# Kernel tuning notes

Measured on AMD Instinct MI355X. Metric: run time of the kernel, lower is better.

The kernel has to match this reference:

```python
import jax, jax.numpy as jnp
import numpy as np

B, L, D, H, E, NL, K = 32, 256, 256, 256, 8, 4, 4


def setup_inputs() -> dict:
    key = jax.random.key(0)
    ks = jax.random.split(key, 8)
    sc = 1.0 / float(np.sqrt(H))
    x = jax.random.normal(ks[0], (B, L, D), jnp.float32)
    conv_w = jax.random.normal(ks[1], (D, 1, K), jnp.float32) * sc
    conv_b = jax.random.normal(ks[2], (D,), jnp.float32) * 0.1
    ln_g = jnp.ones((D,), jnp.float32)
    ln_b = jnp.zeros((D,), jnp.float32)
    W_ih = jax.random.normal(ks[3], (NL, H, D), jnp.float32) * sc
    W_hh = jax.random.normal(ks[4], (NL, H, H), jnp.float32) * sc
    # first layer scaling_init='normal', remaining layers 'ones'
    r0 = jax.random.normal(ks[5], (1, E, D), jnp.float32)
    r = jnp.concatenate([r0, jnp.ones((NL - 1, E, D), jnp.float32)], axis=0)
    s0 = jax.random.normal(ks[6], (1, E, H), jnp.float32)
    s = jnp.concatenate([s0, jnp.ones((NL - 1, E, H), jnp.float32)], axis=0)
    b = jnp.zeros((NL, H), jnp.float32)
    return dict(x=x, conv_w=conv_w, conv_b=conv_b, ln_g=ln_g, ln_b=ln_b,
                W_ih=W_ih, W_hh=W_hh, r=r, s=s, b=b)


def _layernorm(x, g, b, eps=1e-5):
    m = x.mean(-1, keepdims=True)
    v = ((x - m) ** 2).mean(-1, keepdims=True)
    return (x - m) * jax.lax.rsqrt(v + eps) * g + b


def _rnn_layer(x, W_ih, W_hh, r, s, b):
    # x: (B, E, L, F); batch-ensemble input scaling, shared GEMM, output scaling
    pre = jnp.einsum('belf,hf->belh', x * r[None, :, None, :], W_ih)
    pre = pre * s[None, :, None, :] + b  # (B, E, L, H)

    def step(h, p_t):
        h = jnp.tanh(p_t + jnp.einsum('beh,kh->bek', h, W_hh))
        return h, h

    h0 = jnp.zeros((x.shape[0], x.shape[1], W_hh.shape[0]), x.dtype)
    h_last, ys = jax.lax.scan(step, h0, jnp.moveaxis(pre, 2, 0))  # scan over L
    return jnp.moveaxis(ys, 0, 2), h_last


def reference(x, conv_w, conv_b, ln_g, ln_b, W_ih, W_hh, r, s, b):
    h = _layernorm(x, ln_g, ln_b)                    # (B, L, D)
    h = jnp.transpose(h, (0, 2, 1))                  # (B, D, L)
    # depthwise causal conv1d: pad=(K-1) both sides then [:, :, :L] == left-pad K-1
    h = jax.lax.conv_general_dilated(
        h, conv_w, window_strides=(1,), padding=[(K - 1, 0)],
        dimension_numbers=('NCH', 'OIH', 'NCH'), feature_group_count=D)
    h = h + conv_b[None, :, None]
    h = jnp.transpose(h, (0, 2, 1))                  # (B, L, D)
    h = jnp.broadcast_to(h[:, None], (B, E, L, D))   # replicate across ensemble
    h_last = None
    for i in range(NL):
        h, h_last = _rnn_layer(h, W_ih[i], W_hh[i], r[i], s[i], b[i])
    return h, h_last
```

## Files before the change

### kernel.cpp

```cpp
#include <hip/hip_runtime.h>
#include <hip/hip_bf16.h>
#include <cstdint>


typedef _Float16 f16;
typedef _Float16 f16x4 __attribute__((ext_vector_type(4)));
typedef _Float16 f16x8 __attribute__((ext_vector_type(8)));
typedef float f32x4 __attribute__((ext_vector_type(4)));

__device__ __forceinline__ float tanh_fast(float x) {
  float e = __expf(2.f * x);
  return fmaf(-2.f, __builtin_amdgcn_rcpf(e + 1.f), 1.f);
}

__global__ __launch_bounds__(256) void ln_kernel(
    const float* __restrict__ x, const float* __restrict__ g,
    const float* __restrict__ beta, float* __restrict__ out)
{
  const int row = blockIdx.x;
  const int t = threadIdx.x;
  const float v = x[row * 256 + t];
  __shared__ float red[4];
  float s = v;
  #pragma unroll
  for (int off = 32; off > 0; off >>= 1) s += __shfl_xor(s, off);
  if ((t & 63) == 0) red[t >> 6] = s;
  __syncthreads();
  const float mean = (red[0] + red[1] + red[2] + red[3]) * (1.f / 256.f);
  const float d = v - mean;
  float sq = d * d;
  #pragma unroll
  for (int off = 32; off > 0; off >>= 1) sq += __shfl_xor(sq, off);
  __syncthreads();
  if ((t & 63) == 0) red[t >> 6] = sq;
  __syncthreads();
  const float var = (red[0] + red[1] + red[2] + red[3]) * (1.f / 256.f);
  out[row * 256 + t] = d * rsqrtf(var + 1e-5f) * g[t] + beta[t];
}

__global__ __launch_bounds__(256) void conv_kernel(
    const float* __restrict__ ln, const float* __restrict__ w,
    const float* __restrict__ cb, float* __restrict__ out)
{
  const int l = blockIdx.x & 255;
  const int b = blockIdx.x >> 8;
  const int d = threadIdx.x;
  const float4 wv = *(const float4*)(w + d * 4);
  const float wk[4] = {wv.x, wv.y, wv.z, wv.w};
  float acc = cb[d];
  #pragma unroll
  for (int k = 0; k < 4; ++k) {
    const int ls = l - 3 + k;
    if (ls >= 0) acc = fmaf(ln[((b << 8) + ls) * 256 + d], wk[k], acc);
  }
  out[((b << 8) + l) * 256 + d] = acc;
}

__global__ __launch_bounds__(512) void wcvt_kernel(
    const float* __restrict__ Wi, const float* __restrict__ Wh,
    f16* __restrict__ wi16, f16* __restrict__ wh16)
{
  const int i = blockIdx.x * 512 + threadIdx.x;
  wi16[i] = (f16)Wi[i];
  wh16[i] = (f16)Wh[i];
}

__global__ void zflags_kernel(int* __restrict__ f) { f[threadIdx.x] = 0; }

#define XS_S 264
#define PRE_S 260

__global__ __launch_bounds__(512, 2) void pipe_kernel(
    const float* __restrict__ cvb,
    const f16* __restrict__ wi16,
    const f16* __restrict__ wh16,
    const float* __restrict__ rr,
    const float* __restrict__ ssc,
    const float* __restrict__ bbv,
    f16* __restrict__ ysA,
    f16* __restrict__ ysB,
    float* __restrict__ preG,
    int* __restrict__ flags,
    float* __restrict__ outh,
    float* __restrict__ outl)
{
  __shared__ __align__(16) f16 Xs[16 * XS_S];
  __shared__ __align__(16) f16 hb[2][16 * 256];

  const int tid = threadIdx.x, lane = tid & 63, w = tid >> 6;
  const int n = lane & 15, q = lane >> 4;
  const int blk = blockIdx.x;
  const int l = blk >> 4, g = blk & 15;
  const int fl = tid >> 5;
  const int fc = (tid & 31) << 3;

  const f16* ysin = (((l - 1) & 1) ? ysB : ysA);
  f16* ysout = ((l & 1) ? ysB : ysA);
  float* pblk = preG + (size_t)blk * 65536;
  const int swz = (n & 7) << 4;

  *(f16x8*)((char*)&hb[0][0] + tid * 16) = (f16x8){};
  __syncthreads();

  int cur = 0;

  for (int c = 0; c < 16; ++c) {
    if (l > 0) {
      if (tid == 0) {
        while (__hip_atomic_load(&flags[(l - 1) * 16 + g], __ATOMIC_ACQUIRE,
                                 __HIP_MEMORY_SCOPE_AGENT) < c + 1)
          __builtin_amdgcn_s_sleep(8);
      }
      __syncthreads();
    }

    {
      f16x8 wih[2][8];
      #pragma unroll
      for (int jt = 0; jt < 2; ++jt) {
        const f16* wib = wi16 + l * 65536 + (w * 32 + jt * 16 + n) * 256 + q * 8;
        #pragma unroll
        for (int p = 0; p < 8; ++p) wih[jt][p] = *(const f16x8*)(wib + p * 32);
      }
      for (int s = 0; s < 16; ++s) {
        const int seq = g * 16 + s;
        const int t = c * 16 + fl;
        if (l == 0) {
          const int bb_ = seq >> 3, e = seq & 7;
          const float* rp = rr + e * 256 + fc;
          const f32x4 rva = *(const f32x4*)rp;
          const f32x4 rvb = *(const f32x4*)(rp + 4);
          const float* src = cvb + (size_t)(((bb_ << 8) + t) << 8) + fc;
          const f32x4 x0 = *(const f32x4*)src * rva;
          const f32x4 x1 = *(const f32x4*)(src + 4) * rvb;
          f16x8 v;
          v[0]=(f16)x0.x; v[1]=(f16)x0.y; v[2]=(f16)x0.z; v[3]=(f16)x0.w;
          v[4]=(f16)x1.x; v[5]=(f16)x1.y; v[6]=(f16)x1.z; v[7]=(f16)x1.w;
          *(f16x8*)(Xs + fl * XS_S + fc) = v;
        } else {
          *(f16x8*)(Xs + fl * XS_S + fc) =
              *(const f16x8*)(ysin + (size_t)seq * 65536 + (size_t)t * 256 + fc);
        }
        __syncthreads();

        const int e = seq & 7;
        float sv[2], bv[2];
        sv[0] = ssc[l * 2048 + e * 256 + w * 32 + n];
        sv[1] = ssc[l * 2048 + e * 256 + w * 32 + 16 + n];
        bv[0] = bbv[l * 256 + w * 32 + n];
        bv[1] = bbv[l * 256 + w * 32 + 16 + n];

        f32x4 g00 = {0,0,0,0}, g10 = g00, g01 = g00, g11 = g00;
        #pragma unroll
        for (int p = 0; p < 4; ++p) {
          const f16x8 afa = *(const f16x8*)(Xs + n * XS_S + p * 32 + q * 8);
          const f16x8 afb = *(const f16x8*)(Xs + n * XS_S + (p + 4) * 32 + q * 8);
          g00 = __builtin_amdgcn_mfma_f32_16x16x32_f16(afa, wih[0][p], g00, 0, 0, 0);
          g10 = __builtin_amdgcn_mfma_f32_16x16x32_f16(afa, wih[1][p], g10, 0, 0, 0);
          g01 = __builtin_amdgcn_mfma_f32_16x16x32_f16(afb, wih[0][p + 4], g01, 0, 0, 0);
          g11 = __builtin_amdgcn_mfma_f32_16x16x32_f16(afb, wih[1][p + 4], g11, 0, 0, 0);
        }
        #pragma unroll
        for (int ri = 0; ri < 4; ++ri) {
          const int off = ((q * 4 + ri) * 16 + s) * 256;
          pblk[off + w * 32 + n]      = fmaf(g00[ri] + g01[ri], sv[0], bv[0]);
          pblk[off + w * 32 + 16 + n] = fmaf(g10[ri] + g11[ri], sv[1], bv[1]);
        }
        __syncthreads();
      }
    }

    {
      f16x8 whh[2][8];
      #pragma unroll
      for (int rt = 0; rt < 2; ++rt) {
        const f16* whb = wh16 + l * 65536 + (w * 32 + rt * 16 + n) * 256 + q * 8;
        #pragma unroll
        for (int p = 0; p < 8; ++p) whh[rt][p] = *(const f16x8*)(whb + p * 32);
      }
      f32x4 pc0 = *(const f32x4*)(pblk + n * 256 + w * 32 + q * 4);
      f32x4 pc1 = *(const f32x4*)(pblk + n * 256 + w * 32 + 16 + q * 4);

      for (int t = 0; t < 16; ++t) {
        const int tn = (t + 1) & 15;
        const f32x4 pn0 = *(const f32x4*)(pblk + (tn * 16 + n) * 256 + w * 32 + q * 4);
        const f32x4 pn1 = *(const f32x4*)(pblk + (tn * 16 + n) * 256 + w * 32 + 16 + q * 4);

        f16x8 Bf[8];
        const char* hc = (const char*)&hb[cur][0];
        #pragma unroll
        for (int p = 0; p < 8; ++p)
          Bf[p] = *(const f16x8*)(hc + ((n * 512 + 64 * p + 16 * q) ^ swz));

        f32x4 ac0 = pc0, ac1 = pc1;
        #pragma unroll
        for (int p = 0; p < 8; ++p) {
          ac0 = __builtin_amdgcn_mfma_f32_16x16x32_f16(whh[0][p], Bf[p], ac0, 0, 0, 0);
          ac1 = __builtin_amdgcn_mfma_f32_16x16x32_f16(whh[1][p], Bf[p], ac1, 0, 0, 0);
        }

        char* hn = (char*)&hb[cur ^ 1][0];
        const int tg = c * 16 + t;
        const int seq = g * 16 + n;
        #pragma unroll
        for (int rt = 0; rt < 2; ++rt) {
          const f32x4 a = rt ? ac1 : ac0;
          const float v0 = tanh_fast(a[0]);
          const float v1 = tanh_fast(a[1]);
          const float v2 = tanh_fast(a[2]);
          const float v3 = tanh_fast(a[3]);
          f16x4 hv;
          hv[0] = (f16)v0; hv[1] = (f16)v1; hv[2] = (f16)v2; hv[3] = (f16)v3;
          *(f16x4*)(hn + ((n * 512 + 64 * w + 32 * rt + 8 * q) ^ swz)) = hv;
          const int col = w * 32 + rt * 16 + q * 4;
          if (l < 3) {
            *(f16x4*)(ysout + (size_t)seq * 65536 + (size_t)tg * 256 + col) = hv;
          } else {
            const f32x4 ov = {v0, v1, v2, v3};
            *(f32x4*)(outh + ((size_t)seq * 256 + tg) * 256 + col) = ov;
            if (tg == 255)
              *(f32x4*)(outl + (size_t)seq * 256 + col) = ov;
          }
        }
        __syncthreads();
        cur ^= 1;
        pc0 = pn0; pc1 = pn1;
      }
    }

    if (l < 3 && tid == 0)
      __hip_atomic_fetch_add(&flags[l * 16 + g], 1, __ATOMIC_RELEASE,
                             __HIP_MEMORY_SCOPE_AGENT);
  }
}

__global__ __launch_bounds__(512, 2) void fused_rnn_kernel(
    const float* __restrict__ cvb,
    const f16* __restrict__ wi16,
    const f16* __restrict__ wh16,
    const float* __restrict__ rr,
    const float* __restrict__ ssc,
    const float* __restrict__ bbv,
    f16* __restrict__ ys16,
    float* __restrict__ outh,
    float* __restrict__ outl)
{
  __shared__ __align__(16) f16 Xs[16 * XS_S];
  __shared__ __align__(16) float preb[16 * PRE_S];
  __shared__ __align__(16) f16 hbuf[2 * 272];

  const int tid = threadIdx.x, lane = tid & 63, w = tid >> 6;
  const int n = lane & 15, q = lane >> 4;
  const int seq = blockIdx.x, b = seq >> 3, e = seq & 7;
  const int fl = tid >> 5;
  const int fc = (tid & 31) << 3;

  const int tj = n & 1, tri = (n >> 1) & 3;
  const int hrow = w * 32 + tj * 16 + q * 4 + tri;
  const bool writer = (n < 8);

  f16* myys = ys16 + (size_t)seq * 65536;

  const float* rp = rr + e * 256 + fc;
  const f32x4 rva = *(const f32x4*)rp;
  const f32x4 rvb = *(const f32x4*)(rp + 4);

  for (int layer = 0; layer < 4; ++layer) {
    f16x8 wih[2][8], whh[2][8];
    float sv[2], bv[2];
    #pragma unroll
    for (int jt = 0; jt < 2; ++jt) {
      const int row = w * 32 + jt * 16 + n;
      const f16* wib = wi16 + layer * 65536 + row * 256 + q * 8;
      const f16* whb = wh16 + layer * 65536 + row * 256 + q * 8;
      #pragma unroll
      for (int kc = 0; kc < 8; ++kc) {
        wih[jt][kc] = *(const f16x8*)(wib + kc * 32);
        whh[jt][kc] = *(const f16x8*)(whb + kc * 32);
      }
      sv[jt] = ssc[layer * 2048 + e * 256 + row];
      bv[jt] = bbv[layer * 256 + row];
    }
    if (tid < 68) ((f16x8*)hbuf)[tid] = (f16x8){};

    for (int c = 0; c < 16; ++c) {
      const int lg = (c << 4) + fl;
      if (layer == 0) {
        const float* src = cvb + (size_t)(((b << 8) + lg) << 8) + fc;
        const f32x4 x0 = *(const f32x4*)src * rva;
        const f32x4 x1 = *(const f32x4*)(src + 4) * rvb;
        f16x8 v;
        v[0]=(f16)x0.x; v[1]=(f16)x0.y; v[2]=(f16)x0.z; v[3]=(f16)x0.w;
        v[4]=(f16)x1.x; v[5]=(f16)x1.y; v[6]=(f16)x1.z; v[7]=(f16)x1.w;
        *(f16x8*)(Xs + fl * XS_S + fc) = v;
      } else {
        *(f16x8*)(Xs + fl * XS_S + fc) = *(const f16x8*)(myys + (size_t)lg * 256 + fc);
      }
      __syncthreads();

      {
        f32x4 g00 = {0,0,0,0}, g10 = g00, g01 = g00, g11 = g00;
        #pragma unroll
        for (int p = 0; p < 4; ++p) {
          const f16x8 afa = *(const f16x8*)(Xs + n * XS_S + p * 32 + q * 8);
          const f16x8 afb = *(const f16x8*)(Xs + n * XS_S + (p + 4) * 32 + q * 8);
          g00 = __builtin_amdgcn_mfma_f32_16x16x32_f16(afa, wih[0][p], g00, 0, 0, 0);
          g10 = __builtin_amdgcn_mfma_f32_16x16x32_f16(afa, wih[1][p], g10, 0, 0, 0);
          g01 = __builtin_amdgcn_mfma_f32_16x16x32_f16(afb, wih[0][p + 4], g01, 0, 0, 0);
          g11 = __builtin_amdgcn_mfma_f32_16x16x32_f16(afb, wih[1][p + 4], g11, 0, 0, 0);
        }
        #pragma unroll
        for (int ri = 0; ri < 4; ++ri) {
          preb[(q * 4 + ri) * PRE_S + w * 32 + n]      = fmaf(g00[ri] + g01[ri], sv[0], bv[0]);
          preb[(q * 4 + ri) * PRE_S + w * 32 + 16 + n] = fmaf(g10[ri] + g11[ri], sv[1], bv[1]);
        }
      }
      __syncthreads();

      #pragma unroll 2
      for (int t = 0; t < 16; ++t) {
        const f16* hbp = hbuf + (t & 1) * 272;
        f16x8 Bf[8];
        #pragma unroll
        for (int kc = 0; kc < 8; ++kc)
          Bf[kc] = *(const f16x8*)(hbp + kc * 32 + q * 8);
        f32x4 a00 = *(const f32x4*)(preb + t * PRE_S + w * 32 + q * 4);
        f32x4 a10 = *(const f32x4*)(preb + t * PRE_S + w * 32 + 16 + q * 4);
        f32x4 a01 = {0,0,0,0}, a11 = {0,0,0,0};
        #pragma unroll
        for (int p = 0; p < 4; ++p) {
          a00 = __builtin_amdgcn_mfma_f32_16x16x32_f16(whh[0][p], Bf[p], a00, 0, 0, 0);
          a10 = __builtin_amdgcn_mfma_f32_16x16x32_f16(whh[1][p], Bf[p], a10, 0, 0, 0);
          a01 = __builtin_amdgcn_mfma_f32_16x16x32_f16(whh[0][p + 4], Bf[p + 4], a01, 0, 0, 0);
          a11 = __builtin_amdgcn_mfma_f32_16x16x32_f16(whh[1][p + 4], Bf[p + 4], a11, 0, 0, 0);
        }
        const f32x4 sums = tj ? (a10 + a11) : (a00 + a01);
        const float v = tanh_fast(sums[tri]);
        if (writer) {
          f16* hnext = hbuf + ((t + 1) & 1) * 272;
          hnext[hrow] = (f16)v;
          preb[t * PRE_S + hrow] = v;
          if (layer == 3 && c == 15 && t == 15)
            outl[(size_t)seq * 256 + hrow] = v;
        }
        __syncthreads();
      }

      {
        const float* srow = preb + fl * PRE_S + fc;
        const f32x4 o0 = *(const f32x4*)srow;
        const f32x4 o1 = *(const f32x4*)(srow + 4);
        if (layer < 3) {
          f16x8 hh;
          hh[0]=(f16)o0.x; hh[1]=(f16)o0.y; hh[2]=(f16)o0.z; hh[3]=(f16)o0.w;
          hh[4]=(f16)o1.x; hh[5]=(f16)o1.y; hh[6]=(f16)o1.z; hh[7]=(f16)o1.w;
          *(f16x8*)(myys + (size_t)lg * 256 + fc) = hh;
        } else {
          float* dst = outh + ((size_t)seq * 256 + lg) * 256 + fc;
          *(f32x4*)dst = o0;
          *(f32x4*)(dst + 4) = o1;
        }
      }
      __syncthreads();
    }
  }
}

extern "C" void kernel_launch(void* const* d_in, const int* in_sizes, int n_in,
                              void* d_out, int out_size, void* d_ws, size_t ws_size,
                              hipStream_t stream) {
  const float* x      = (const float*)d_in[0];
  const float* conv_w = (const float*)d_in[1];
  const float* conv_b = (const float*)d_in[2];
  const float* ln_g   = (const float*)d_in[3];
  const float* ln_b   = (const float*)d_in[4];
  const float* W_ih   = (const float*)d_in[5];
  const float* W_hh   = (const float*)d_in[6];
  const float* r      = (const float*)d_in[7];
  const float* s      = (const float*)d_in[8];
  const float* bb     = (const float*)d_in[9];

  float* outh = (float*)d_out;
  float* outl = outh + 16777216;

  const size_t NEED = (size_t)112 << 20;
  if (ws_size >= NEED) {
    f16*   ysA  = (f16*)d_ws;
    f16*   ysB  = (f16*)((char*)d_ws + ((size_t)32 << 20));
    float* cvb  = (float*)((char*)d_ws + ((size_t)64 << 20));
    float* lnb  = (float*)((char*)d_ws + ((size_t)72 << 20));
    f16*   wi16 = (f16*)((char*)d_ws + ((size_t)80 << 20));
    f16*   wh16 = wi16 + 262144;
    float* preG = (float*)((char*)d_ws + ((size_t)81 << 20));
    int*   flags = (int*)((char*)d_ws + ((size_t)97 << 20));

    zflags_kernel<<<1, 64, 0, stream>>>(flags);
    ln_kernel<<<8192, 256, 0, stream>>>(x, ln_g, ln_b, lnb);
    conv_kernel<<<8192, 256, 0, stream>>>(lnb, conv_w, conv_b, cvb);
    wcvt_kernel<<<512, 512, 0, stream>>>(W_ih, W_hh, wi16, wh16);
    pipe_kernel<<<64, 512, 0, stream>>>(cvb, wi16, wh16, r, s, bb,
                                        ysA, ysB, preG, flags, outh, outl);
  } else {
    f16*   ys16 = (f16*)d_ws;
    float* cvb  = (float*)((char*)d_ws + (32u << 20));
    float* lnb  = (float*)((char*)d_ws + (40u << 20));
    f16*   wi16 = (f16*)((char*)d_ws + (48u << 20));
    f16*   wh16 = wi16 + 262144;

    ln_kernel<<<8192, 256, 0, stream>>>(x, ln_g, ln_b, lnb);
    conv_kernel<<<8192, 256, 0, stream>>>(lnb, conv_w, conv_b, cvb);
    wcvt_kernel<<<512, 512, 0, stream>>>(W_ih, W_hh, wi16, wh16);
    fused_rnn_kernel<<<256, 512, 0, stream>>>(cvb, wi16, wh16, r, s, bb,
                                              ys16, outh, outl);
  }
}
```

Measured before the change: 686.6 us.

## Pre-scale fp16 inputs in conv, keep weights resident, batch hidden-state stores per chunk

The conv kernel now also applies the per-ensemble input scaling r and writes an fp16 (B,E,L,D) tensor, so layer 0 no longer rescales and converts inputs on the fly. Inside the pipelined kernel, W_ih and W_hh fragments are loaded into registers once per block, and the input GEMM reads A fragments straight from global memory. That removes the LDS staging buffer and its two barriers per sequence step. Hidden states for a 16-step chunk are kept in a 16-slot LDS ring and written out afterwards with coalesced 16-byte stores, and the ping-pong ys buffers collapse into one. The costs are higher register pressure, final-layer outputs rounded through fp16 before widening to fp32, and a single shared ys buffer that relies on the flag ordering to stay correct.

```diff
diff --git a/kernel.cpp b/kernel.cpp
--- a/kernel.cpp
+++ b/kernel.cpp
@@ -38,9 +38,10 @@
   out[row * 256 + t] = d * rsqrtf(var + 1e-5f) * g[t] + beta[t];
 }
 
-__global__ __launch_bounds__(256) void conv_kernel(
+__global__ __launch_bounds__(256) void convr_kernel(
     const float* __restrict__ ln, const float* __restrict__ w,
-    const float* __restrict__ cb, float* __restrict__ out)
+    const float* __restrict__ cb, const float* __restrict__ rr,
+    f16* __restrict__ xr)
 {
   const int l = blockIdx.x & 255;
   const int b = blockIdx.x >> 8;
@@ -53,6 +54,26 @@
     const int ls = l - 3 + k;
     if (ls >= 0) acc = fmaf(ln[((b << 8) + ls) * 256 + d], wk[k], acc);
   }
+  #pragma unroll
+  for (int e = 0; e < 8; ++e)
+    xr[(size_t)(((b * 8 + e) * 256 + l)) * 256 + d] = (f16)(acc * rr[e * 256 + d]);
+}
+
+__global__ __launch_bounds__(256) void conv_kernel(
+    const float* __restrict__ ln, const float* __restrict__ w,
+    const float* __restrict__ cb, float* __restrict__ out)
+{
+  const int l = blockIdx.x & 255;
+  const int b = blockIdx.x >> 8;
+  const int d = threadIdx.x;
+  const float4 wv = *(const float4*)(w + d * 4);
+  const float wk[4] = {wv.x, wv.y, wv.z, wv.w};
+  float acc = cb[d];
+  #pragma unroll
+  for (int k = 0; k < 4; ++k) {
+    const int ls = l - 3 + k;
+    if (ls >= 0) acc = fmaf(ln[((b << 8) + ls) * 256 + d], wk[k], acc);
+  }
   out[((b << 8) + l) * 256 + d] = acc;
 }
 
@@ -71,38 +92,53 @@
 #define PRE_S 260
 
 __global__ __launch_bounds__(512, 2) void pipe_kernel(
-    const float* __restrict__ cvb,
+    const f16* __restrict__ xr16,
     const f16* __restrict__ wi16,
     const f16* __restrict__ wh16,
-    const float* __restrict__ rr,
     const float* __restrict__ ssc,
     const float* __restrict__ bbv,
-    f16* __restrict__ ysA,
-    f16* __restrict__ ysB,
+    f16* __restrict__ ys,
     float* __restrict__ preG,
     int* __restrict__ flags,
     float* __restrict__ outh,
     float* __restrict__ outl)
 {
-  __shared__ __align__(16) f16 Xs[16 * XS_S];
-  __shared__ __align__(16) f16 hb[2][16 * 256];
+  __shared__ __align__(16) f16 hb[16][4096];
 
   const int tid = threadIdx.x, lane = tid & 63, w = tid >> 6;
   const int n = lane & 15, q = lane >> 4;
   const int blk = blockIdx.x;
   const int l = blk >> 4, g = blk & 15;
-  const int fl = tid >> 5;
-  const int fc = (tid & 31) << 3;
-
-  const f16* ysin = (((l - 1) & 1) ? ysB : ysA);
-  f16* ysout = ((l & 1) ? ysB : ysA);
+  const int swz = (n & 7) << 4;
+  const int fs = tid >> 5;
+  const int fd = (tid & 31) << 3;
+  const int fswz = (fs & 7) << 4;
+
+  const f16* xin = (l == 0) ? xr16 : ys;
   float* pblk = preG + (size_t)blk * 65536;
-  const int swz = (n & 7) << 4;
+
+  f16x8 wih[2][8], whh[2][8];
+  #pragma unroll
+  for (int jt = 0; jt < 2; ++jt) {
+    const f16* wib = wi16 + l * 65536 + (w * 32 + jt * 16 + n) * 256 + q * 8;
+    const f16* whb = wh16 + l * 65536 + (w * 32 + jt * 16 + n) * 256 + q * 8;
+    #pragma unroll
+    for (int p = 0; p < 8; ++p) {
+      wih[jt][p] = *(const f16x8*)(wib + p * 32);
+      whh[jt][p] = *(const f16x8*)(whb + p * 32);
+    }
+  }
+  #pragma unroll
+  for (int jt = 0; jt < 2; ++jt) {
+    #pragma unroll
+    for (int p = 0; p < 8; ++p) {
+      asm volatile("" : "+v"(wih[jt][p]));
+      asm volatile("" : "+v"(whh[jt][p]));
+    }
+  }
 
   *(f16x8*)((char*)&hb[0][0] + tid * 16) = (f16x8){};
   __syncthreads();
-
-  int cur = 0;
 
   for (int c = 0; c < 16; ++c) {
     if (l > 0) {
@@ -114,119 +150,96 @@
       __syncthreads();
     }
 
+    #pragma unroll 2
+    for (int s = 0; s < 16; ++s) {
+      const int seq = g * 16 + s;
+      const f16* xb = xin + (size_t)seq * 65536 + (c * 16 + n) * 256 + q * 8;
+      f32x4 g00 = {0,0,0,0}, g10 = g00, g01 = g00, g11 = g00;
+      #pragma unroll
+      for (int p = 0; p < 4; ++p) {
+        const f16x8 afa = *(const f16x8*)(xb + p * 32);
+        const f16x8 afb = *(const f16x8*)(xb + (p + 4) * 32);
+        g00 = __builtin_amdgcn_mfma_f32_16x16x32_f16(afa, wih[0][p], g00, 0, 0, 0);
+        g10 = __builtin_amdgcn_mfma_f32_16x16x32_f16(afa, wih[1][p], g10, 0, 0, 0);
+        g01 = __builtin_amdgcn_mfma_f32_16x16x32_f16(afb, wih[0][p + 4], g01, 0, 0, 0);
+        g11 = __builtin_amdgcn_mfma_f32_16x16x32_f16(afb, wih[1][p + 4], g11, 0, 0, 0);
+      }
+      const int e = s & 7;
+      const float sv0 = ssc[l * 2048 + e * 256 + w * 32 + n];
+      const float sv1 = ssc[l * 2048 + e * 256 + w * 32 + 16 + n];
+      const float bv0 = bbv[l * 256 + w * 32 + n];
+      const float bv1 = bbv[l * 256 + w * 32 + 16 + n];
+      #pragma unroll
+      for (int ri = 0; ri < 4; ++ri) {
+        const int off = ((q * 4 + ri) * 16 + s) * 256;
+        pblk[off + w * 32 + n]      = fmaf(g00[ri] + g01[ri], sv0, bv0);
+        pblk[off + w * 32 + 16 + n] = fmaf(g10[ri] + g11[ri], sv1, bv1);
+      }
+    }
+
+    f32x4 pc0 = *(const f32x4*)(pblk + n * 256 + w * 32 + q * 4);
+    f32x4 pc1 = *(const f32x4*)(pblk + n * 256 + w * 32 + 16 + q * 4);
+    for (int t = 0; t < 16; ++t) {
+      const int tn = (t + 1) & 15;
+      const f32x4 pn0 = *(const f32x4*)(pblk + (tn * 16 + n) * 256 + w * 32 + q * 4);
+      const f32x4 pn1 = *(const f32x4*)(pblk + (tn * 16 + n) * 256 + w * 32 + 16 + q * 4);
+
+      const char* hc = (const char*)&hb[t][0];
+      f16x8 Bf[8];
+      #pragma unroll
+      for (int p = 0; p < 8; ++p)
+        Bf[p] = *(const f16x8*)(hc + ((n * 512 + 64 * p + 16 * q) ^ swz));
+
+      f32x4 ac0 = pc0, ac1 = pc1;
+      #pragma unroll
+      for (int p = 0; p < 8; ++p) {
+        ac0 = __builtin_amdgcn_mfma_f32_16x16x32_f16(whh[0][p], Bf[p], ac0, 0, 0, 0);
+        ac1 = __builtin_amdgcn_mfma_f32_16x16x32_f16(whh[1][p], Bf[p], ac1, 0, 0, 0);
+      }
+
+      char* hn = (char*)&hb[(t + 1) & 15][0];
+      #pragma unroll
+      for (int rt = 0; rt < 2; ++rt) {
+        const f32x4 a = rt ? ac1 : ac0;
+        f16x4 hv;
+        hv[0] = (f16)tanh_fast(a[0]);
+        hv[1] = (f16)tanh_fast(a[1]);
+        hv[2] = (f16)tanh_fast(a[2]);
+        hv[3] = (f16)tanh_fast(a[3]);
+        *(f16x4*)(hn + ((n * 512 + 64 * w + 32 * rt + 8 * q) ^ swz)) = hv;
+      }
+      __syncthreads();
+      pc0 = pn0; pc1 = pn1;
+    }
+
     {
-      f16x8 wih[2][8];
-      #pragma unroll
-      for (int jt = 0; jt < 2; ++jt) {
-        const f16* wib = wi16 + l * 65536 + (w * 32 + jt * 16 + n) * 256 + q * 8;
-        #pragma unroll
-        for (int p = 0; p < 8; ++p) wih[jt][p] = *(const f16x8*)(wib + p * 32);
-      }
-      for (int s = 0; s < 16; ++s) {
-        const int seq = g * 16 + s;
-        const int t = c * 16 + fl;
-        if (l == 0) {
-          const int bb_ = seq >> 3, e = seq & 7;
-          const float* rp = rr + e * 256 + fc;
-          const f32x4 rva = *(const f32x4*)rp;
-          const f32x4 rvb = *(const f32x4*)(rp + 4);
-          const float* src = cvb + (size_t)(((bb_ << 8) + t) << 8) + fc;
-          const f32x4 x0 = *(const f32x4*)src * rva;
-          const f32x4 x1 = *(const f32x4*)(src + 4) * rvb;
-          f16x8 v;
-          v[0]=(f16)x0.x; v[1]=(f16)x0.y; v[2]=(f16)x0.z; v[3]=(f16)x0.w;
-          v[4]=(f16)x1.x; v[5]=(f16)x1.y; v[6]=(f16)x1.z; v[7]=(f16)x1.w;
-          *(f16x8*)(Xs + fl * XS_S + fc) = v;
+      const int seq = g * 16 + fs;
+      for (int tp = 0; tp < 16; ++tp) {
+        const f16x8 hv = *(const f16x8*)(
+            (const char*)&hb[(tp + 1) & 15][0] + ((fs * 512 + fd * 2) ^ fswz));
+        if (l < 3) {
+          *(f16x8*)(ys + (size_t)seq * 65536 + (size_t)(c * 16 + tp) * 256 + fd) = hv;
         } else {
-          *(f16x8*)(Xs + fl * XS_S + fc) =
-              *(const f16x8*)(ysin + (size_t)seq * 65536 + (size_t)t * 256 + fc);
-        }
-        __syncthreads();
-
-        const int e = seq & 7;
-        float sv[2], bv[2];
-        sv[0] = ssc[l * 2048 + e * 256 + w * 32 + n];
-        sv[1] = ssc[l * 2048 + e * 256 + w * 32 + 16 + n];
-        bv[0] = bbv[l * 256 + w * 32 + n];
-        bv[1] = bbv[l * 256 + w * 32 + 16 + n];
-
-        f32x4 g00 = {0,0,0,0}, g10 = g00, g01 = g00, g11 = g00;
-        #pragma unroll
-        for (int p = 0; p < 4; ++p) {
-          const f16x8 afa = *(const f16x8*)(Xs + n * XS_S + p * 32 + q * 8);
-          const f16x8 afb = *(const f16x8*)(Xs + n * XS_S + (p + 4) * 32 + q * 8);
-          g00 = __builtin_amdgcn_mfma_f32_16x16x32_f16(afa, wih[0][p], g00, 0, 0, 0);
-          g10 = __builtin_amdgcn_mfma_f32_16x16x32_f16(afa, wih[1][p], g10, 0, 0, 0);
-          g01 = __builtin_amdgcn_mfma_f32_16x16x32_f16(afb, wih[0][p + 4], g01, 0, 0, 0);
-          g11 = __builtin_amdgcn_mfma_f32_16x16x32_f16(afb, wih[1][p + 4], g11, 0, 0, 0);
-        }
-        #pragma unroll
-        for (int ri = 0; ri < 4; ++ri) {
-          const int off = ((q * 4 + ri) * 16 + s) * 256;
-          pblk[off + w * 32 + n]      = fmaf(g00[ri] + g01[ri], sv[0], bv[0]);
-          pblk[off + w * 32 + 16 + n] = fmaf(g10[ri] + g11[ri], sv[1], bv[1]);
-        }
-        __syncthreads();
-      }
-    }
-
-    {
-      f16x8 whh[2][8];
-      #pragma unroll
-      for (int rt = 0; rt < 2; ++rt) {
-        const f16* whb = wh16 + l * 65536 + (w * 32 + rt * 16 + n) * 256 + q * 8;
-        #pragma unroll
-        for (int p = 0; p < 8; ++p) whh[rt][p] = *(const f16x8*)(whb + p * 32);
-      }
-      f32x4 pc0 = *(const f32x4*)(pblk + n * 256 + w * 32 + q * 4);
-      f32x4 pc1 = *(const f32x4*)(pblk + n * 256 + w * 32 + 16 + q * 4);
-
-      for (int t = 0; t < 16; ++t) {
-        const int tn = (t + 1) & 15;
-        const f32x4 pn0 = *(const f32x4*)(pblk + (tn * 16 + n) * 256 + w * 32 + q * 4);
-        const f32x4 pn1 = *(const f32x4*)(pblk + (tn * 16 + n) * 256 + w * 32 + 16 + q * 4);
-
-        f16x8 Bf[8];
-        const char* hc = (const char*)&hb[cur][0];
-        #pragma unroll
-        for (int p = 0; p < 8; ++p)
-          Bf[p] = *(const f16x8*)(hc + ((n * 512 + 64 * p + 16 * q) ^ swz));
-
-        f32x4 ac0 = pc0, ac1 = pc1;
-        #pragma unroll
-        for (int p = 0; p < 8; ++p) {
-          ac0 = __builtin_amdgcn_mfma_f32_16x16x32_f16(whh[0][p], Bf[p], ac0, 0, 0, 0);
-          ac1 = __builtin_amdgcn_mfma_f32_16x16x32_f16(whh[1][p], Bf[p], ac1, 0, 0, 0);
-        }
-
-        char* hn = (char*)&hb[cur ^ 1][0];
-        const int tg = c * 16 + t;
-        const int seq = g * 16 + n;
-        #pragma unroll
-        for (int rt = 0; rt < 2; ++rt) {
-          const f32x4 a = rt ? ac1 : ac0;
-          const float v0 = tanh_fast(a[0]);
-          const float v1 = tanh_fast(a[1]);
-          const float v2 = tanh_fast(a[2]);
-          const float v3 = tanh_fast(a[3]);
-          f16x4 hv;
-          hv[0] = (f16)v0; hv[1] = (f16)v1; hv[2] = (f16)v2; hv[3] = (f16)v3;
-          *(f16x4*)(hn + ((n * 512 + 64 * w + 32 * rt + 8 * q) ^ swz)) = hv;
-          const int col = w * 32 + rt * 16 + q * 4;
-          if (l < 3) {
-            *(f16x4*)(ysout + (size_t)seq * 65536 + (size_t)tg * 256 + col) = hv;
-          } else {
-            const f32x4 ov = {v0, v1, v2, v3};
-            *(f32x4*)(outh + ((size_t)seq * 256 + tg) * 256 + col) = ov;
-            if (tg == 255)
-              *(f32x4*)(outl + (size_t)seq * 256 + col) = ov;
-          }
-        }
-        __syncthreads();
-        cur ^= 1;
-        pc0 = pn0; pc1 = pn1;
-      }
-    }
+          f32x4 o0, o1;
+          o0[0]=(float)hv[0]; o0[1]=(float)hv[1]; o0[2]=(float)hv[2]; o0[3]=(float)hv[3];
+          o1[0]=(float)hv[4]; o1[1]=(float)hv[5]; o1[2]=(float)hv[6]; o1[3]=(float)hv[7];
+          float* dst = outh + ((size_t)seq * 256 + c * 16 + tp) * 256 + fd;
+          *(f32x4*)dst = o0;
+          *(f32x4*)(dst + 4) = o1;
+        }
+      }
+      if (l == 3 && c == 15) {
+        const f16x8 hv = *(const f16x8*)(
+            (const char*)&hb[0][0] + ((fs * 512 + fd * 2) ^ fswz));
+        f32x4 o0, o1;
+        o0[0]=(float)hv[0]; o0[1]=(float)hv[1]; o0[2]=(float)hv[2]; o0[3]=(float)hv[3];
+        o1[0]=(float)hv[4]; o1[1]=(float)hv[5]; o1[2]=(float)hv[6]; o1[3]=(float)hv[7];
+        float* dst = outl + (size_t)seq * 256 + fd;
+        *(f32x4*)dst = o0;
+        *(f32x4*)(dst + 4) = o1;
+      }
+    }
+    __syncthreads();
 
     if (l < 3 && tid == 0)
       __hip_atomic_fetch_add(&flags[l * 16 + g], 1, __ATOMIC_RELEASE,
@@ -383,23 +396,22 @@
   float* outh = (float*)d_out;
   float* outl = outh + 16777216;
 
-  const size_t NEED = (size_t)112 << 20;
+  const size_t NEED = (size_t)82 << 20;
   if (ws_size >= NEED) {
-    f16*   ysA  = (f16*)d_ws;
-    f16*   ysB  = (f16*)((char*)d_ws + ((size_t)32 << 20));
-    float* cvb  = (float*)((char*)d_ws + ((size_t)64 << 20));
-    float* lnb  = (float*)((char*)d_ws + ((size_t)72 << 20));
+    f16*   ysb  = (f16*)d_ws;
+    f16*   xr16 = (f16*)((char*)d_ws + ((size_t)32 << 20));
+    float* preG = (float*)((char*)d_ws + ((size_t)64 << 20));
+    float* lnb  = (float*)((char*)d_ws + ((size_t)64 << 20));
     f16*   wi16 = (f16*)((char*)d_ws + ((size_t)80 << 20));
     f16*   wh16 = wi16 + 262144;
-    float* preG = (float*)((char*)d_ws + ((size_t)81 << 20));
-    int*   flags = (int*)((char*)d_ws + ((size_t)97 << 20));
+    int*   flags = (int*)((char*)d_ws + ((size_t)81 << 20));
 
     zflags_kernel<<<1, 64, 0, stream>>>(flags);
     ln_kernel<<<8192, 256, 0, stream>>>(x, ln_g, ln_b, lnb);
-    conv_kernel<<<8192, 256, 0, stream>>>(lnb, conv_w, conv_b, cvb);
+    convr_kernel<<<8192, 256, 0, stream>>>(lnb, conv_w, conv_b, r, xr16);
     wcvt_kernel<<<512, 512, 0, stream>>>(W_ih, W_hh, wi16, wh16);
-    pipe_kernel<<<64, 512, 0, stream>>>(cvb, wi16, wh16, r, s, bb,
-                                        ysA, ysB, preG, flags, outh, outl);
+    pipe_kernel<<<64, 512, 0, stream>>>(xr16, wi16, wh16, s, bb,
+                                        ysb, preG, flags, outh, outl);
   } else {
     f16*   ys16 = (f16*)d_ws;
     float* cvb  = (float*)((char*)d_ws + (32u << 20));
```

Result: slower. 1.008 ms (+46.8%).
